# Kernel tuning notes

Measured on AMD Instinct MI355X. Metric: run time of the kernel, lower is better.

## Reference

```python
import jax, jax.numpy as jnp
import numpy as np

B, T, I, H = 64, 2048, 256, 256


def setup_inputs() -> dict:
    key = jax.random.key(0)
    ks = jax.random.split(key, 9)
    s = 1.0 / np.sqrt(H).astype(np.float32)  # torch nn.RNN init: U(-1/sqrt(H), 1/sqrt(H))
    u = lambda k, shape: jax.random.uniform(k, shape, jnp.float32, -s, s)
    return {
        "input_feature": jax.random.normal(ks[0], (B, T, I), jnp.float32),
        "W_ih0": u(ks[1], (H, I)),
        "W_hh0": u(ks[2], (H, H)),
        "b_ih0": u(ks[3], (H,)),
        "b_hh0": u(ks[4], (H,)),
        "W_ih1": u(ks[5], (H, H)),
        "W_hh1": u(ks[6], (H, H)),
        "b_ih1": u(ks[7], (H,)),
        "b_hh1": u(ks[8], (H,)),
    }


def _rnn_layer(x, W_ih, W_hh, b_ih, b_hh):
    # x: [B, T, F]. Precompute the input projection for all timesteps at once,
    # then scan the recurrence: h_t = tanh(x_t W_ih^T + b_ih + h_{t-1} W_hh^T + b_hh)
    pre = jnp.einsum("btf,hf->bth", x, W_ih) + b_ih + b_hh  # [B, T, H]
    h0 = jnp.zeros((x.shape[0], W_hh.shape[0]), x.dtype)

    def step(h, p):
        h_new = jnp.tanh(p + h @ W_hh.T)
        return h_new, h_new

    _, ys = jax.lax.scan(step, h0, jnp.swapaxes(pre, 0, 1))  # [T, B, H]
    return jnp.swapaxes(ys, 0, 1)  # [B, T, H]


def reference(input_feature, W_ih0, W_hh0, b_ih0, b_hh0, W_ih1, W_hh1, b_ih1, b_hh1):
    # hidden_0 = zeros, batch_first=True, tanh nonlinearity (torch.nn.RNN default)
    h = _rnn_layer(input_feature, W_ih0, W_hh0, b_ih0, b_hh0)
    h = _rnn_layer(h, W_ih1, W_hh1, b_ih1, b_hh1)
    return h  # output: [B, T, H] (module returns only `output`)
```

## Files before the change

kernel.cpp:

```cpp
#include <hip/hip_runtime.h>
#include <stdint.h>

#define B_ 64
#define T_ 2048
#define H_ 256
#define S_ 64
#define C_ (T_ / S_)

typedef unsigned int u32;
typedef unsigned short u16;
typedef __attribute__((ext_vector_type(8))) short short8;
typedef __attribute__((ext_vector_type(4))) float f32x4;

#define SWZ(row, byte) (((row) * 512) + ((byte) ^ (((row) & 7) << 4)))

static __device__ __forceinline__ u32 cvtpk(float a, float b) {
  u32 d;
  asm("v_cvt_pk_bf16_f32 %0, %1, %2" : "=v"(d) : "v"(a), "v"(b));
  return d;
}
static __device__ __forceinline__ uint4 pack8(float4 a, float4 b) {
  uint4 r;
  r.x = cvtpk(a.x, a.y); r.y = cvtpk(a.z, a.w);
  r.z = cvtpk(b.x, b.y); r.w = cvtpk(b.z, b.w);
  return r;
}
static __device__ __forceinline__ short8 as8(uint4 v) {
  return __builtin_bit_cast(short8, v);
}
static __device__ __forceinline__ f32x4 mfma4(uint4 a, uint4 b, f32x4 c) {
  return __builtin_amdgcn_mfma_f32_16x16x32_bf16(as8(a), as8(b), c, 0, 0, 0);
}
static __device__ __forceinline__ float fast_tanh(float x) {
  float e = __expf(2.0f * x);
  float r = __builtin_amdgcn_rcpf(e + 1.0f);
  return fmaf(-2.0f, r, 1.0f);
}

template <int NQ>
static __device__ __forceinline__ void load_wfrag(const float* W, int qbase, int bl,
                                                  int g, uint4 wf[NQ][8]) {
#pragma unroll
  for (int q = 0; q < NQ; ++q) {
    const float* wr = W + (size_t)((qbase + q) * 16 + bl) * H_ + g * 8;
#pragma unroll
    for (int kc = 0; kc < 8; ++kc) {
      float4 a = *(const float4*)(wr + kc * 32);
      float4 b = *(const float4*)(wr + kc * 32 + 4);
      wf[q][kc] = pack8(a, b);
    }
  }
}

static __device__ __forceinline__ void wait_ge(u32* f, u32 tgt) {
  if (__hip_atomic_load(f, __ATOMIC_ACQUIRE, __HIP_MEMORY_SCOPE_AGENT) >= tgt) return;
  while (__hip_atomic_load(f, __ATOMIC_ACQUIRE, __HIP_MEMORY_SCOPE_AGENT) < tgt)
    __builtin_amdgcn_s_sleep(8);
}
static __device__ __forceinline__ void drain_all() {
  asm volatile("s_waitcnt vmcnt(0) lgkmcnt(0)" ::: "memory");
  __builtin_amdgcn_s_barrier();
}
static __device__ __forceinline__ void publish_val(u32* f, u32 v) {
  drain_all();
  if (threadIdx.x == 0)
    __hip_atomic_store(f, v, __ATOMIC_RELEASE, __HIP_MEMORY_SCOPE_AGENT);
}
static __device__ __forceinline__ void publish_add(u32* f) {
  drain_all();
  if (threadIdx.x == 0)
    (void)__hip_atomic_fetch_add(f, 1u, __ATOMIC_RELEASE, __HIP_MEMORY_SCOPE_AGENT);
}

__global__ void init_flags(u32* f) { f[threadIdx.x] = 0; }

static __device__ void proj0_body(char* smem, const float* X, const float* Wih0,
                                  const float* bih0, const float* bhh0,
                                  float* dout, int ch, int bid2,
                                  const uint4 wf[2][8], const float4 cb[2]) {
  const int tid = threadIdx.x;
  const int lane = tid & 63, wv = tid >> 6;
  const int bl = lane & 15, g = lane >> 4;
  char* sb0 = smem;
  char* sb1 = smem + 8192;

  const int sr = tid >> 5, sc8 = (tid & 31) * 8;
  auto rowbase = [&](int it) -> size_t {
    const int b = bid2 * 2 + (it >> 2), i = it & 3;
    return (size_t)(b * T_ + ch * S_ + i * 16);
  };
  float4 s0, s1;
  {
    const float4* xs = (const float4*)(X + (rowbase(0) + sr) * H_ + sc8);
    s0 = xs[0]; s1 = xs[1];
  }
  for (int it = 0; it < 8; ++it) {
    char* sb = (it & 1) ? sb1 : sb0;
    *(uint4*)(sb + SWZ(sr, sc8 * 2)) = pack8(s0, s1);
    __syncthreads();
    if (it + 1 < 8) {
      const float4* xn = (const float4*)(X + (rowbase(it + 1) + sr) * H_ + sc8);
      s0 = xn[0]; s1 = xn[1];
    }
    uint4 hf[8];
#pragma unroll
    for (int kc = 0; kc < 8; ++kc)
      hf[kc] = *(const uint4*)(sb + SWZ(bl, kc * 64 + g * 16));
    f32x4 acc[2];
#pragma unroll
    for (int q = 0; q < 2; ++q) {
      acc[q] = (f32x4){0.f, 0.f, 0.f, 0.f};
#pragma unroll
      for (int kc = 0; kc < 8; ++kc)
        acc[q] = mfma4(wf[q][kc], hf[kc], acc[q]);
    }
    float* od = dout + (rowbase(it) + bl) * H_;
#pragma unroll
    for (int q = 0; q < 2; ++q) {
      const int j0 = (wv * 2 + q) * 16 + g * 4;
      float4 o;
      o.x = acc[q][0] + cb[q].x; o.y = acc[q][1] + cb[q].y;
      o.z = acc[q][2] + cb[q].z; o.w = acc[q][3] + cb[q].w;
      *(float4*)(od + j0) = o;
    }
    __syncthreads();
  }
}

__global__ __launch_bounds__(256, 2) void pre_mfma(const float* X, const float* W,
                                                   const float* bi, const float* bh,
                                                   float* P, int tpw) {
  __shared__ char sb_[2][8192];
  const int tid = threadIdx.x;
  const int lane = tid & 63, wv = tid >> 6;
  const int bl = lane & 15, g = lane >> 4;

  uint4 wf[4][8];
  load_wfrag<4>(W, wv * 4, bl, g, wf);
  float4 bias[4];
#pragma unroll
  for (int q = 0; q < 4; ++q) {
    const int j0 = (wv * 4 + q) * 16 + g * 4;
    float4 a = *(const float4*)(bi + j0);
    float4 c = *(const float4*)(bh + j0);
    bias[q].x = a.x + c.x; bias[q].y = a.y + c.y;
    bias[q].z = a.z + c.z; bias[q].w = a.w + c.w;
  }
  const size_t row0 = (size_t)blockIdx.x * tpw * 16;
  const int sr = tid >> 4, sc = (tid & 15) * 16;
  float4 s0, s1, s2, s3;
  {
    const float4* xs = (const float4*)(X + (row0 + sr) * H_ + sc);
    s0 = xs[0]; s1 = xs[1]; s2 = xs[2]; s3 = xs[3];
  }
  for (int i = 0; i < tpw; ++i) {
    char* sb = sb_[i & 1];
    *(uint4*)(sb + SWZ(sr, sc * 2)) = pack8(s0, s1);
    *(uint4*)(sb + SWZ(sr, sc * 2 + 16)) = pack8(s2, s3);
    __syncthreads();
    if (i + 1 < tpw) {
      const float4* xn = (const float4*)(X + (row0 + (i + 1) * 16 + sr) * H_ + sc);
      s0 = xn[0]; s1 = xn[1]; s2 = xn[2]; s3 = xn[3];
    }
    uint4 hf[8];
#pragma unroll
    for (int kc = 0; kc < 8; ++kc)
      hf[kc] = *(const uint4*)(sb + SWZ(bl, kc * 64 + g * 16));
    f32x4 acc[4];
#pragma unroll
    for (int q = 0; q < 4; ++q) {
      acc[q] = (f32x4){0.f, 0.f, 0.f, 0.f};
#pragma unroll
      for (int kc = 0; kc < 8; ++kc)
        acc[q] = mfma4(wf[q][kc], hf[kc], acc[q]);
    }
#pragma unroll
    for (int q = 0; q < 4; ++q) {
      const int j0 = (wv * 4 + q) * 16 + g * 4;
      float4 o;
      o.x = acc[q][0] + bias[q].x; o.y = acc[q][1] + bias[q].y;
      o.z = acc[q][2] + bias[q].z; o.w = acc[q][3] + bias[q].w;
      *(float4*)(P + (row0 + i * 16 + bl) * H_ + j0) = o;
    }
    __syncthreads();
  }
}

__global__ __launch_bounds__(512, 1) void rec_mfma(const float* pre, const float* W,
                                                   float* out) {
  __shared__ char hb_[2][8192];
  const int tid = threadIdx.x;
  const int lane = tid & 63, wv = tid >> 6;
  const int bl = lane & 15, g = lane >> 4;
  const int b0 = blockIdx.x * 16;

  uint4 wf[2][8];
  load_wfrag<2>(W, wv * 2, bl, g, wf);
  {
    uint4 z = make_uint4(0, 0, 0, 0);
    ((uint4*)hb_[0])[tid] = z;
    ((uint4*)hb_[1])[tid] = z;
  }
  const float* prow = pre + (size_t)(b0 + bl) * T_ * H_;
  float* orow = out + (size_t)(b0 + bl) * T_ * H_;
  float4 pr0[2], pr1[2];
#pragma unroll
  for (int q = 0; q < 2; ++q) {
    const int j0 = (wv * 2 + q) * 16 + g * 4;
    pr0[q] = *(const float4*)(prow + 0 * H_ + j0);
    pr1[q] = *(const float4*)(prow + 1 * H_ + j0);
  }
  __syncthreads();

  auto step = [&](int t, float4 (&pr)[2], char* rbuf, char* wbuf) {
    uint4 hf[8];
#pragma unroll
    for (int kc = 0; kc < 8; ++kc)
      hf[kc] = *(const uint4*)(rbuf + SWZ(bl, kc * 64 + g * 16));
    f32x4 accA[2], accB[2];
#pragma unroll
    for (int q = 0; q < 2; ++q) {
      accA[q] = (f32x4){0.f, 0.f, 0.f, 0.f};
      accB[q] = (f32x4){0.f, 0.f, 0.f, 0.f};
#pragma unroll
      for (int kc = 0; kc < 4; ++kc) {
        accA[q] = mfma4(wf[q][kc], hf[kc], accA[q]);
        accB[q] = mfma4(wf[q][kc + 4], hf[kc + 4], accB[q]);
      }
    }
#pragma unroll
    for (int q = 0; q < 2; ++q) {
      const int j0 = (wv * 2 + q) * 16 + g * 4;
      const float* pq = (const float*)&pr[q];
      float v0 = fast_tanh(accA[q][0] + accB[q][0] + pq[0]);
      float v1 = fast_tanh(accA[q][1] + accB[q][1] + pq[1]);
      float v2 = fast_tanh(accA[q][2] + accB[q][2] + pq[2]);
      float v3 = fast_tanh(accA[q][3] + accB[q][3] + pq[3]);
      uint2 hw; hw.x = cvtpk(v0, v1); hw.y = cvtpk(v2, v3);
      *(uint2*)(wbuf + SWZ(bl, j0 * 2)) = hw;
      float4 o; o.x = v0; o.y = v1; o.z = v2; o.w = v3;
      *(float4*)(orow + (size_t)t * H_ + j0) = o;
      if (t + 2 < T_)
        pr[q] = *(const float4*)(prow + (size_t)(t + 2) * H_ + j0);
    }
    asm volatile("s_waitcnt lgkmcnt(0)" ::: "memory");
    __builtin_amdgcn_s_barrier();
    __builtin_amdgcn_sched_barrier(0);
  };
  for (int t = 0; t < T_; t += 2) {
    step(t, pr0, hb_[0], hb_[1]);
    step(t + 1, pr1, hb_[1], hb_[0]);
  }
}

__global__ __launch_bounds__(512, 1) void persist_k(
    const float* X, float* dout,
    const float* Wih0, const float* bih0, const float* bhh0, const float* Whh0,
    const float* Wih1, const float* Whh1, const float* bih1, const float* bhh1,
    u16* ring, u32* flags) {
  __shared__ __align__(16) char smem[2 * 8192];
  const int tid = threadIdx.x;
  const int lane = tid & 63, wv = tid >> 6;
  const int bl = lane & 15, g = lane >> 4;
  const int bid = blockIdx.x;
  char* sb0 = smem;
  char* sb1 = smem + 8192;
  u32* proj0_cnt = flags;
  auto rec0_prog = [&](int p) { return flags + 32 + 32 * p; };
  auto proj1_prog = [&](int p) { return flags + 160 + 32 * p; };

  if (bid < 4) {
    const int p = bid;
    uint4 wf[2][8];
    load_wfrag<2>(Whh0, wv * 2, bl, g, wf);
    { uint4 z = make_uint4(0, 0, 0, 0); ((uint4*)sb0)[tid] = z; }
    __syncthreads();
    const float* prow = dout + (size_t)(p * 16 + bl) * T_ * H_;
    u16* rb = ring + (size_t)(p * 16 + bl) * H_;

    for (int c = 0; c < C_; ++c) {
      const u32 ptgt = 32u * (u32)((c + 2 < C_) ? (c + 2) : C_);
      wait_ge(proj0_cnt, ptgt);
      if (c >= 1) wait_ge(proj1_prog(p), (u32)(c - 1));
      const float* pch = prow + (size_t)c * S_ * H_;
      u16* rch = rb + ((size_t)(c & 1) * S_) * (B_ * H_);
      float4 pr0[2], pr1[2];
#pragma unroll
      for (int q = 0; q < 2; ++q) {
        const int j0 = (wv * 2 + q) * 16 + g * 4;
        pr0[q] = *(const float4*)(pch + 0 * H_ + j0);
        pr1[q] = *(const float4*)(pch + 1 * H_ + j0);
      }
      auto step = [&](int s, float4 (&pr)[2], char* rbuf, char* wbuf) {
        uint4 hf[8];
#pragma unroll
        for (int kc = 0; kc < 8; ++kc)
          hf[kc] = *(const uint4*)(rbuf + SWZ(bl, kc * 64 + g * 16));
        f32x4 accA[2], accB[2];
#pragma unroll
        for (int q = 0; q < 2; ++q) {
          accA[q] = (f32x4){0.f, 0.f, 0.f, 0.f};
          accB[q] = (f32x4){0.f, 0.f, 0.f, 0.f};
#pragma unroll
          for (int kc = 0; kc < 4; ++kc) {
            accA[q] = mfma4(wf[q][kc], hf[kc], accA[q]);
            accB[q] = mfma4(wf[q][kc + 4], hf[kc + 4], accB[q]);
          }
        }
#pragma unroll
        for (int q = 0; q < 2; ++q) {
          const int j0 = (wv * 2 + q) * 16 + g * 4;
          const float* pq = (const float*)&pr[q];
          float v0 = fast_tanh(accA[q][0] + accB[q][0] + pq[0]);
          float v1 = fast_tanh(accA[q][1] + accB[q][1] + pq[1]);
          float v2 = fast_tanh(accA[q][2] + accB[q][2] + pq[2]);
          float v3 = fast_tanh(accA[q][3] + accB[q][3] + pq[3]);
          uint2 hw; hw.x = cvtpk(v0, v1); hw.y = cvtpk(v2, v3);
          *(uint2*)(wbuf + SWZ(bl, j0 * 2)) = hw;
          *(uint2*)(rch + (size_t)s * (B_ * H_) + j0) = hw;
          if (s + 2 < S_)
            pr[q] = *(const float4*)(pch + (size_t)(s + 2) * H_ + j0);
        }
        asm volatile("s_waitcnt lgkmcnt(0)" ::: "memory");
        __builtin_amdgcn_s_barrier();
        __builtin_amdgcn_sched_barrier(0);
      };
      for (int s = 0; s < S_; s += 2) {
        step(s, pr0, sb0, sb1);
        step(s + 1, pr1, sb1, sb0);
      }
      publish_val(rec0_prog(p), (u32)(c + 1));
    }
  } else if (bid < 8) {
    const int p = bid - 4;
    uint4 wf[2][8];
    load_wfrag<2>(Wih1, wv * 2, bl, g, wf);
    float4 cb[2];
#pragma unroll
    for (int q = 0; q < 2; ++q) {
      const int j0 = (wv * 2 + q) * 16 + g * 4;
      float4 a = *(const float4*)(bih1 + j0);
      float4 b = *(const float4*)(bhh1 + j0);
      cb[q].x = a.x + b.x; cb[q].y = a.y + b.y;
      cb[q].z = a.z + b.z; cb[q].w = a.w + b.w;
    }
    const int sr = tid >> 5, scb = (tid & 31) * 16;
    for (int ch = 0; ch < C_; ++ch) {
      wait_ge(rec0_prog(p), (u32)(ch + 1));
      const u16* rbase2 = ring + ((size_t)(ch & 1) * S_) * (B_ * H_) + (size_t)p * 16 * H_;
      uint4 v = *(const uint4*)(rbase2 + (size_t)sr * H_ + (tid & 31) * 8);
      for (int s = 0; s < S_; ++s) {
        char* sb = (s & 1) ? sb1 : sb0;
        *(uint4*)(sb + SWZ(sr, scb)) = v;
        __syncthreads();
        if (s + 1 < S_)
          v = *(const uint4*)(rbase2 + (size_t)(s + 1) * (B_ * H_) + (size_t)sr * H_ + (tid & 31) * 8);
        uint4 hf[8];
#pragma unroll
        for (int kc = 0; kc < 8; ++kc)
          hf[kc] = *(const uint4*)(sb + SWZ(bl, kc * 64 + g * 16));
        f32x4 acc[2];
#pragma unroll
        for (int q = 0; q < 2; ++q) {
          acc[q] = (f32x4){0.f, 0.f, 0.f, 0.f};
#pragma unroll
          for (int kc = 0; kc < 8; ++kc)
            acc[q] = mfma4(wf[q][kc], hf[kc], acc[q]);
        }
        float* od = dout + (size_t)(p * 16 + bl) * T_ * H_ + (size_t)(ch * S_ + s) * H_;
#pragma unroll
        for (int q = 0; q < 2; ++q) {
          const int j0 = (wv * 2 + q) * 16 + g * 4;
          float4 o;
          o.x = acc[q][0] + cb[q].x; o.y = acc[q][1] + cb[q].y;
          o.z = acc[q][2] + cb[q].z; o.w = acc[q][3] + cb[q].w;
          *(float4*)(od + j0) = o;
        }
        __syncthreads();
      }
      publish_val(proj1_prog(p), (u32)(ch + 1));
    }
  } else if (bid < 12) {
    const int p = bid - 8;
    uint4 wf[2][8];
    load_wfrag<2>(Whh1, wv * 2, bl, g, wf);
    { uint4 z = make_uint4(0, 0, 0, 0); ((uint4*)sb0)[tid] = z; }
    __syncthreads();
    float* prow = dout + (size_t)(p * 16 + bl) * T_ * H_;

    for (int ch = 0; ch < C_; ++ch) {
      wait_ge(proj1_prog(p), (u32)(ch + 1));
      float* pch = prow + (size_t)ch * S_ * H_;
      float4 pr0[2], pr1[2];
#pragma unroll
      for (int q = 0; q < 2; ++q) {
        const int j0 = (wv * 2 + q) * 16 + g * 4;
        pr0[q] = *(const float4*)(pch + 0 * H_ + j0);
        pr1[q] = *(const float4*)(pch + 1 * H_ + j0);
      }
      auto step = [&](int s, float4 (&pr)[2], char* rbuf, char* wbuf) {
        uint4 hf[8];
#pragma unroll
        for (int kc = 0; kc < 8; ++kc)
          hf[kc] = *(const uint4*)(rbuf + SWZ(bl, kc * 64 + g * 16));
        f32x4 accA[2], accB[2];
#pragma unroll
        for (int q = 0; q < 2; ++q) {
          accA[q] = (f32x4){0.f, 0.f, 0.f, 0.f};
          accB[q] = (f32x4){0.f, 0.f, 0.f, 0.f};
#pragma unroll
          for (int kc = 0; kc < 4; ++kc) {
            accA[q] = mfma4(wf[q][kc], hf[kc], accA[q]);
            accB[q] = mfma4(wf[q][kc + 4], hf[kc + 4], accB[q]);
          }
        }
#pragma unroll
        for (int q = 0; q < 2; ++q) {
          const int j0 = (wv * 2 + q) * 16 + g * 4;
          const float* pq = (const float*)&pr[q];
          float v0 = fast_tanh(accA[q][0] + accB[q][0] + pq[0]);
          float v1 = fast_tanh(accA[q][1] + accB[q][1] + pq[1]);
          float v2 = fast_tanh(accA[q][2] + accB[q][2] + pq[2]);
          float v3 = fast_tanh(accA[q][3] + accB[q][3] + pq[3]);
          uint2 hw; hw.x = cvtpk(v0, v1); hw.y = cvtpk(v2, v3);
          *(uint2*)(wbuf + SWZ(bl, j0 * 2)) = hw;
          float4 o; o.x = v0; o.y = v1; o.z = v2; o.w = v3;
          *(float4*)(pch + (size_t)s * H_ + j0) = o;
          if (s + 2 < S_)
            pr[q] = *(const float4*)(pch + (size_t)(s + 2) * H_ + j0);
        }
        asm volatile("s_waitcnt lgkmcnt(0)" ::: "memory");
        __builtin_amdgcn_s_barrier();
        __builtin_amdgcn_sched_barrier(0);
      };
      for (int s = 0; s < S_; s += 2) {
        step(s, pr0, sb0, sb1);
        step(s + 1, pr1, sb1, sb0);
      }
    }
  } else {
    const int b2 = bid - 12;
    uint4 wf[2][8];
    load_wfrag<2>(Wih0, wv * 2, bl, g, wf);
    float4 cb[2];
#pragma unroll
    for (int q = 0; q < 2; ++q) {
      const int j0 = (wv * 2 + q) * 16 + g * 4;
      float4 a = *(const float4*)(bih0 + j0);
      float4 b = *(const float4*)(bhh0 + j0);
      cb[q].x = a.x + b.x; cb[q].y = a.y + b.y;
      cb[q].z = a.z + b.z; cb[q].w = a.w + b.w;
    }
    for (int c = 0; c < C_; ++c) {
      proj0_body(smem, X, Wih0, bih0, bhh0, dout, c, b2, wf, cb);
      publish_add(proj0_cnt);
    }
  }
}

extern "C" void kernel_launch(void* const* d_in, const int* in_sizes, int n_in,
                              void* d_out, int out_size, void* d_ws, size_t ws_size,
                              hipStream_t stream) {
  (void)in_sizes; (void)n_in; (void)out_size;
  const float* x    = (const float*)d_in[0];
  const float* Wih0 = (const float*)d_in[1];
  const float* Whh0 = (const float*)d_in[2];
  const float* bih0 = (const float*)d_in[3];
  const float* bhh0 = (const float*)d_in[4];
  const float* Wih1 = (const float*)d_in[5];
  const float* Whh1 = (const float*)d_in[6];
  const float* bih1 = (const float*)d_in[7];
  const float* bhh1 = (const float*)d_in[8];
  float* out = (float*)d_out;

  const size_t ring_bytes = (size_t)2 * S_ * B_ * H_ * sizeof(u16);
  const size_t need = 4096 + ring_bytes;

  if (ws_size >= need) {
    u32* flags = (u32*)d_ws;
    u16* ring = (u16*)((char*)d_ws + 4096);
    init_flags<<<dim3(1), dim3(1024), 0, stream>>>(flags);
    persist_k<<<dim3(44), dim3(512), 0, stream>>>(
        x, out, Wih0, bih0, bhh0, Whh0, Wih1, Whh1, bih1, bhh1, ring, flags);
  } else {
    const int TPW = 8;
    const int NWG = (B_ * T_) / (TPW * 16);
    pre_mfma<<<dim3(NWG), dim3(256), 0, stream>>>(x, Wih0, bih0, bhh0, out, TPW);
    rec_mfma<<<dim3(B_ / 16), dim3(512), 0, stream>>>(out, Whh0, out);
    pre_mfma<<<dim3(NWG), dim3(256), 0, stream>>>(out, Wih1, bih1, bhh1, out, TPW);
    rec_mfma<<<dim3(B_ / 16), dim3(512), 0, stream>>>(out, Whh1, out);
  }
}
```

Measured before the change: 2.154 ms.

## Halve pipeline chunk size and fold bias and projection into MFMA accumulators

Shrinks the time chunk shared between the projection and recurrence stages from 64 to 32 steps, so the downstream stages can start sooner and the pipeline fill shrinks, at the cost of twice as many flag publishes and waits. The recurrence steps now seed the MFMA accumulator with the precomputed projection, and the projection stages seed it with the bias, which removes the separate add instructions from the serial critical path. tanh now uses v_exp_f32 directly with a prescaled exponent instead of __expf.

```diff
diff --git a/kernel.cpp b/kernel.cpp
--- a/kernel.cpp
+++ b/kernel.cpp
@@ -4,8 +4,9 @@
 #define B_ 64
 #define T_ 2048
 #define H_ 256
-#define S_ 64
+#define S_ 32
 #define C_ (T_ / S_)
+#define NT (S_ / 16)
 
 typedef unsigned int u32;
 typedef unsigned short u16;
@@ -32,7 +33,8 @@
   return __builtin_amdgcn_mfma_f32_16x16x32_bf16(as8(a), as8(b), c, 0, 0, 0);
 }
 static __device__ __forceinline__ float fast_tanh(float x) {
-  float e = __expf(2.0f * x);
+  float e;
+  asm("v_exp_f32 %0, %1" : "=v"(e) : "v"(x * 2.8853900817779268f));
   float r = __builtin_amdgcn_rcpf(e + 1.0f);
   return fmaf(-2.0f, r, 1.0f);
 }
@@ -74,9 +76,8 @@
 
 __global__ void init_flags(u32* f) { f[threadIdx.x] = 0; }
 
-static __device__ void proj0_body(char* smem, const float* X, const float* Wih0,
-                                  const float* bih0, const float* bhh0,
-                                  float* dout, int ch, int bid2,
+static __device__ void proj0_body(char* smem, const float* X, float* dout,
+                                  int ch, int bid2,
                                   const uint4 wf[2][8], const float4 cb[2]) {
   const int tid = threadIdx.x;
   const int lane = tid & 63, wv = tid >> 6;
@@ -86,7 +87,7 @@
 
   const int sr = tid >> 5, sc8 = (tid & 31) * 8;
   auto rowbase = [&](int it) -> size_t {
-    const int b = bid2 * 2 + (it >> 2), i = it & 3;
+    const int b = bid2 * 2 + it / NT, i = it % NT;
     return (size_t)(b * T_ + ch * S_ + i * 16);
   };
   float4 s0, s1;
@@ -94,11 +95,12 @@
     const float4* xs = (const float4*)(X + (rowbase(0) + sr) * H_ + sc8);
     s0 = xs[0]; s1 = xs[1];
   }
-  for (int it = 0; it < 8; ++it) {
+#pragma unroll
+  for (int it = 0; it < 2 * NT; ++it) {
     char* sb = (it & 1) ? sb1 : sb0;
     *(uint4*)(sb + SWZ(sr, sc8 * 2)) = pack8(s0, s1);
     __syncthreads();
-    if (it + 1 < 8) {
+    if (it + 1 < 2 * NT) {
       const float4* xn = (const float4*)(X + (rowbase(it + 1) + sr) * H_ + sc8);
       s0 = xn[0]; s1 = xn[1];
     }
@@ -109,7 +111,7 @@
     f32x4 acc[2];
 #pragma unroll
     for (int q = 0; q < 2; ++q) {
-      acc[q] = (f32x4){0.f, 0.f, 0.f, 0.f};
+      acc[q] = (f32x4){cb[q].x, cb[q].y, cb[q].z, cb[q].w};
 #pragma unroll
       for (int kc = 0; kc < 8; ++kc)
         acc[q] = mfma4(wf[q][kc], hf[kc], acc[q]);
@@ -118,9 +120,7 @@
 #pragma unroll
     for (int q = 0; q < 2; ++q) {
       const int j0 = (wv * 2 + q) * 16 + g * 4;
-      float4 o;
-      o.x = acc[q][0] + cb[q].x; o.y = acc[q][1] + cb[q].y;
-      o.z = acc[q][2] + cb[q].z; o.w = acc[q][3] + cb[q].w;
+      float4 o; o.x = acc[q][0]; o.y = acc[q][1]; o.z = acc[q][2]; o.w = acc[q][3];
       *(float4*)(od + j0) = o;
     }
     __syncthreads();
@@ -220,7 +220,7 @@
     f32x4 accA[2], accB[2];
 #pragma unroll
     for (int q = 0; q < 2; ++q) {
-      accA[q] = (f32x4){0.f, 0.f, 0.f, 0.f};
+      accA[q] = __builtin_bit_cast(f32x4, pr[q]);
       accB[q] = (f32x4){0.f, 0.f, 0.f, 0.f};
 #pragma unroll
       for (int kc = 0; kc < 4; ++kc) {
@@ -231,11 +231,10 @@
 #pragma unroll
     for (int q = 0; q < 2; ++q) {
       const int j0 = (wv * 2 + q) * 16 + g * 4;
-      const float* pq = (const float*)&pr[q];
-      float v0 = fast_tanh(accA[q][0] + accB[q][0] + pq[0]);
-      float v1 = fast_tanh(accA[q][1] + accB[q][1] + pq[1]);
-      float v2 = fast_tanh(accA[q][2] + accB[q][2] + pq[2]);
-      float v3 = fast_tanh(accA[q][3] + accB[q][3] + pq[3]);
+      float v0 = fast_tanh(accA[q][0] + accB[q][0]);
+      float v1 = fast_tanh(accA[q][1] + accB[q][1]);
+      float v2 = fast_tanh(accA[q][2] + accB[q][2]);
+      float v3 = fast_tanh(accA[q][3] + accB[q][3]);
       uint2 hw; hw.x = cvtpk(v0, v1); hw.y = cvtpk(v2, v3);
       *(uint2*)(wbuf + SWZ(bl, j0 * 2)) = hw;
       float4 o; o.x = v0; o.y = v1; o.z = v2; o.w = v3;
@@ -299,7 +298,7 @@
         f32x4 accA[2], accB[2];
 #pragma unroll
         for (int q = 0; q < 2; ++q) {
-          accA[q] = (f32x4){0.f, 0.f, 0.f, 0.f};
+          accA[q] = __builtin_bit_cast(f32x4, pr[q]);
           accB[q] = (f32x4){0.f, 0.f, 0.f, 0.f};
 #pragma unroll
           for (int kc = 0; kc < 4; ++kc) {
@@ -310,11 +309,10 @@
 #pragma unroll
         for (int q = 0; q < 2; ++q) {
           const int j0 = (wv * 2 + q) * 16 + g * 4;
-          const float* pq = (const float*)&pr[q];
-          float v0 = fast_tanh(accA[q][0] + accB[q][0] + pq[0]);
-          float v1 = fast_tanh(accA[q][1] + accB[q][1] + pq[1]);
-          float v2 = fast_tanh(accA[q][2] + accB[q][2] + pq[2]);
-          float v3 = fast_tanh(accA[q][3] + accB[q][3] + pq[3]);
+          float v0 = fast_tanh(accA[q][0] + accB[q][0]);
+          float v1 = fast_tanh(accA[q][1] + accB[q][1]);
+          float v2 = fast_tanh(accA[q][2] + accB[q][2]);
+          float v3 = fast_tanh(accA[q][3] + accB[q][3]);
           uint2 hw; hw.x = cvtpk(v0, v1); hw.y = cvtpk(v2, v3);
           *(uint2*)(wbuf + SWZ(bl, j0 * 2)) = hw;
           *(uint2*)(rch + (size_t)s * (B_ * H_) + j0) = hw;
@@ -362,7 +360,7 @@
         f32x4 acc[2];
 #pragma unroll
         for (int q = 0; q < 2; ++q) {
-          acc[q] = (f32x4){0.f, 0.f, 0.f, 0.f};
+          acc[q] = (f32x4){cb[q].x, cb[q].y, cb[q].z, cb[q].w};
 #pragma unroll
           for (int kc = 0; kc < 8; ++kc)
             acc[q] = mfma4(wf[q][kc], hf[kc], acc[q]);
@@ -371,9 +369,7 @@
 #pragma unroll
         for (int q = 0; q < 2; ++q) {
           const int j0 = (wv * 2 + q) * 16 + g * 4;
-          float4 o;
-          o.x = acc[q][0] + cb[q].x; o.y = acc[q][1] + cb[q].y;
-          o.z = acc[q][2] + cb[q].z; o.w = acc[q][3] + cb[q].w;
+          float4 o; o.x = acc[q][0]; o.y = acc[q][1]; o.z = acc[q][2]; o.w = acc[q][3];
           *(float4*)(od + j0) = o;
         }
         __syncthreads();
@@ -406,7 +402,7 @@
         f32x4 accA[2], accB[2];
 #pragma unroll
         for (int q = 0; q < 2; ++q) {
-          accA[q] = (f32x4){0.f, 0.f, 0.f, 0.f};
+          accA[q] = __builtin_bit_cast(f32x4, pr[q]);
           accB[q] = (f32x4){0.f, 0.f, 0.f, 0.f};
 #pragma unroll
           for (int kc = 0; kc < 4; ++kc) {
@@ -417,11 +413,10 @@
 #pragma unroll
         for (int q = 0; q < 2; ++q) {
           const int j0 = (wv * 2 + q) * 16 + g * 4;
-          const float* pq = (const float*)&pr[q];
-          float v0 = fast_tanh(accA[q][0] + accB[q][0] + pq[0]);
-          float v1 = fast_tanh(accA[q][1] + accB[q][1] + pq[1]);
-          float v2 = fast_tanh(accA[q][2] + accB[q][2] + pq[2]);
-          float v3 = fast_tanh(accA[q][3] + accB[q][3] + pq[3]);
+          float v0 = fast_tanh(accA[q][0] + accB[q][0]);
+          float v1 = fast_tanh(accA[q][1] + accB[q][1]);
+          float v2 = fast_tanh(accA[q][2] + accB[q][2]);
+          float v3 = fast_tanh(accA[q][3] + accB[q][3]);
           uint2 hw; hw.x = cvtpk(v0, v1); hw.y = cvtpk(v2, v3);
           *(uint2*)(wbuf + SWZ(bl, j0 * 2)) = hw;
           float4 o; o.x = v0; o.y = v1; o.z = v2; o.w = v3;
@@ -452,7 +447,7 @@
       cb[q].z = a.z + b.z; cb[q].w = a.w + b.w;
     }
     for (int c = 0; c < C_; ++c) {
-      proj0_body(smem, X, Wih0, bih0, bhh0, dout, c, b2, wf, cb);
+      proj0_body(smem, X, dout, c, b2, wf, cb);
       publish_add(proj0_cnt);
     }
   }
```

After: 2.201 ms. 2.2% more time.
